# Performance work log

Hardware: AMD Instinct MI355X
Metric: run time of the kernel (lower is better)

The kernel has to match this reference:

```python
import jax, jax.numpy as jnp
import numpy as np

D0 = 1.0          # constraint distance d
NPEND = 128       # points per pendulum chain
NB = 1024         # number of chains (= batch.max()+1)
LATENT = 256      # latent dim of y
NDIM = 3          # spatial dimensions; x dim = 2*NDIM (pos + vel)


def setup_inputs() -> dict:
    key = jax.random.key(0)
    k1, k2, k3 = jax.random.split(key, 3)
    N = NB * NPEND
    y = jax.random.normal(k1, (N, LATENT), dtype=jnp.float32)
    z = jax.random.normal(k2, (N,), dtype=jnp.float32)
    K = jax.random.normal(k3, (LATENT, 2 * NDIM), dtype=jnp.float32) * 0.05
    batch = (jnp.arange(N, dtype=jnp.int32) // NPEND).astype(jnp.int32)
    return {"y": y, "z": z, "K": K, "batch": batch}


def _delta_r(r):
    # dr[:,0] = r[:,0]; dr[:,i] = r[:,i] - r[:,i-1]
    return jnp.concatenate([r[:, :1], r[:, 1:] - r[:, :-1]], axis=1)


def reference(y, z, K, batch):
    x = y @ K                                  # [N, 6]
    ndim = x.shape[-1] // 2                    # pos_only=False -> 3
    nb = batch.shape[0] // NPEND               # == batch.max()+1 by construction
    r = x[:, :ndim].reshape(nb, -1, ndim)      # [nb, npend, 3]

    dr = _delta_r(r)                           # [nb, npend, 3]
    drnorm = jnp.linalg.norm(dr, axis=-1)      # [nb, npend]
    c = drnorm - D0                            # constraint values
    rn = dr / drnorm[..., None]                # unit chain-difference vectors

    # Jacobian-transpose times constraints, fused over the chain dimension:
    # out[:,i] = c_i * rn_i - c_{i+1} * rn_{i+1};  out[:,-1] = c_{-1} * rn_{-1}
    t = c[..., None] * rn                      # [nb, npend, 3]
    out = t - jnp.concatenate([t[:, 1:], jnp.zeros_like(t[:, :1])], axis=1)

    lam_x = jnp.zeros_like(x).at[:, :ndim].set(out.reshape(-1, ndim))
    lam_y = lam_x @ K.T                        # [N, latent]
    return lam_y
```

## Files before the change

### kernel.cpp

```cpp
#include <hip/hip_runtime.h>

#define NPEND  128
#define LATENT 256
#define KCOLS  6
#define D0_C   1.0f

__global__ __launch_bounds__(256)
void pend_kernel_f32(const float* __restrict__ y,
                     const float* __restrict__ K,
                     float* __restrict__ out)
{
    __shared__ float sR[NPEND][3];

    const int tid  = threadIdx.x;
    const int wave = tid >> 6;
    const int lane = tid & 63;
    const int hw   = lane >> 5;
    const int hl   = lane & 31;

    float k0[8], k1[8], k2[8];
#pragma unroll
    for (int e = 0; e < 8; ++e) {
        const int l = hl * 8 + e;
        k0[e] = K[l * KCOLS + 0];
        k1[e] = K[l * KCOLS + 1];
        k2[e] = K[l * KCOLS + 2];
    }

    const size_t ybase = (size_t)blockIdx.x * ((size_t)NPEND * LATENT);

    for (int p = wave * 2; p < NPEND; p += 8) {
        const int row = p + hw;
        const float* yr = y + ybase + (size_t)row * LATENT + hl * 8;
        const float4 va = *(const float4*)(yr);
        const float4 vb = *(const float4*)(yr + 4);

        float s0 = va.x*k0[0] + va.y*k0[1] + va.z*k0[2] + va.w*k0[3]
                 + vb.x*k0[4] + vb.y*k0[5] + vb.z*k0[6] + vb.w*k0[7];
        float s1 = va.x*k1[0] + va.y*k1[1] + va.z*k1[2] + va.w*k1[3]
                 + vb.x*k1[4] + vb.y*k1[5] + vb.z*k1[6] + vb.w*k1[7];
        float s2 = va.x*k2[0] + va.y*k2[1] + va.z*k2[2] + va.w*k2[3]
                 + vb.x*k2[4] + vb.y*k2[5] + vb.z*k2[6] + vb.w*k2[7];

#pragma unroll
        for (int off = 16; off > 0; off >>= 1) {
            s0 += __shfl_down(s0, off, 32);
            s1 += __shfl_down(s1, off, 32);
            s2 += __shfl_down(s2, off, 32);
        }
        if (hl == 0) {
            sR[row][0] = s0; sR[row][1] = s1; sR[row][2] = s2;
        }
    }
    __syncthreads();

    for (int p = wave * 2; p < NPEND; p += 8) {
        const int row = p + hw;

        const float rx = sR[row][0], ry = sR[row][1], rz = sR[row][2];
        float px = 0.f, py = 0.f, pz = 0.f;
        if (row > 0) { px = sR[row-1][0]; py = sR[row-1][1]; pz = sR[row-1][2]; }

        const float dx = rx - px, dy = ry - py, dz = rz - pz;
        const float n  = sqrtf(dx*dx + dy*dy + dz*dz);
        const float s  = (n - D0_C) / n;
        float ox = s * dx, oy = s * dy, oz = s * dz;

        if (row < NPEND - 1) {
            const float nx = sR[row+1][0], ny = sR[row+1][1], nz = sR[row+1][2];
            const float ex = nx - rx, ey = ny - ry, ez = nz - rz;
            const float n2 = sqrtf(ex*ex + ey*ey + ez*ez);
            const float t2 = (n2 - D0_C) / n2;
            ox -= t2 * ex; oy -= t2 * ey; oz -= t2 * ez;
        }

        float4 wa, wb;
        wa.x = ox*k0[0] + oy*k1[0] + oz*k2[0];
        wa.y = ox*k0[1] + oy*k1[1] + oz*k2[1];
        wa.z = ox*k0[2] + oy*k1[2] + oz*k2[2];
        wa.w = ox*k0[3] + oy*k1[3] + oz*k2[3];
        wb.x = ox*k0[4] + oy*k1[4] + oz*k2[4];
        wb.y = ox*k0[5] + oy*k1[5] + oz*k2[5];
        wb.z = ox*k0[6] + oy*k1[6] + oz*k2[6];
        wb.w = ox*k0[7] + oy*k1[7] + oz*k2[7];

        float* orow = out + ybase + (size_t)row * LATENT + hl * 8;
        *(float4*)(orow)     = wa;
        *(float4*)(orow + 4) = wb;
    }
}

extern "C" void kernel_launch(void* const* d_in, const int* in_sizes, int n_in,
                              void* d_out, int out_size, void* d_ws, size_t ws_size,
                              hipStream_t stream) {
    const float* y = (const float*)d_in[0];
    const float* K = (const float*)d_in[2];
    float* out = (float*)d_out;

    int N  = (n_in > 1 && in_sizes) ? in_sizes[1] : (1024 * NPEND);
    int nb = N / NPEND;
    if (nb <= 0) nb = 1024;
    (void)out_size; (void)d_ws; (void)ws_size;

    pend_kernel_f32<<<nb, 256, 0, stream>>>(y, K, out);
}
```

Before: 248.3 us.

## Split each pendulum chain across four blocks with halo rows

Each block now processes a 32-row segment of a chain instead of the whole 128-row chain, and recomputes one halo row on each side to get neighbour positions. This quadruples the grid so more blocks are in flight and each block's two phases are shorter. The cost is redundant projection of up to two extra rows per segment, about six percent more reads of y.

```diff
diff --git a/kernel.cpp b/kernel.cpp
--- a/kernel.cpp
+++ b/kernel.cpp
@@ -4,19 +4,26 @@
 #define LATENT 256
 #define KCOLS  6
 #define D0_C   1.0f
+#define SEG    32
+#define SEGS_PER_CHAIN (NPEND / SEG)
 
 __global__ __launch_bounds__(256)
 void pend_kernel_f32(const float* __restrict__ y,
                      const float* __restrict__ K,
                      float* __restrict__ out)
 {
-    __shared__ float sR[NPEND][3];
+    __shared__ float sR[SEG + 2][3];
 
     const int tid  = threadIdx.x;
-    const int wave = tid >> 6;
-    const int lane = tid & 63;
-    const int hw   = lane >> 5;
-    const int hl   = lane & 31;
+    const int hwid = tid >> 5;
+    const int hl   = tid & 31;
+
+    const int chain = blockIdx.x >> 2;
+    const int seg   = blockIdx.x & 3;
+    const int row0  = seg * SEG;
+    const int rlo   = (row0 > 0) ? row0 - 1 : 0;
+    const int rhi   = (row0 + SEG < NPEND) ? row0 + SEG : NPEND - 1;
+    const int nrows = rhi - rlo + 1;
 
     float k0[8], k1[8], k2[8];
 #pragma unroll
@@ -27,11 +34,11 @@
         k2[e] = K[l * KCOLS + 2];
     }
 
-    const size_t ybase = (size_t)blockIdx.x * ((size_t)NPEND * LATENT);
+    const size_t cbase = (size_t)chain * ((size_t)NPEND * LATENT);
 
-    for (int p = wave * 2; p < NPEND; p += 8) {
-        const int row = p + hw;
-        const float* yr = y + ybase + (size_t)row * LATENT + hl * 8;
+    for (int i = hwid; i < nrows; i += 8) {
+        const int row = rlo + i;
+        const float* yr = y + cbase + (size_t)row * LATENT + hl * 8;
         const float4 va = *(const float4*)(yr);
         const float4 vb = *(const float4*)(yr + 4);
 
@@ -49,17 +56,18 @@
             s2 += __shfl_down(s2, off, 32);
         }
         if (hl == 0) {
-            sR[row][0] = s0; sR[row][1] = s1; sR[row][2] = s2;
+            sR[i][0] = s0; sR[i][1] = s1; sR[i][2] = s2;
         }
     }
     __syncthreads();
 
-    for (int p = wave * 2; p < NPEND; p += 8) {
-        const int row = p + hw;
+    for (int i = hwid; i < SEG; i += 8) {
+        const int row = row0 + i;
+        const int si  = row - rlo;
 
-        const float rx = sR[row][0], ry = sR[row][1], rz = sR[row][2];
+        const float rx = sR[si][0], ry = sR[si][1], rz = sR[si][2];
         float px = 0.f, py = 0.f, pz = 0.f;
-        if (row > 0) { px = sR[row-1][0]; py = sR[row-1][1]; pz = sR[row-1][2]; }
+        if (row > 0) { px = sR[si-1][0]; py = sR[si-1][1]; pz = sR[si-1][2]; }
 
         const float dx = rx - px, dy = ry - py, dz = rz - pz;
         const float n  = sqrtf(dx*dx + dy*dy + dz*dz);
@@ -67,7 +75,7 @@
         float ox = s * dx, oy = s * dy, oz = s * dz;
 
         if (row < NPEND - 1) {
-            const float nx = sR[row+1][0], ny = sR[row+1][1], nz = sR[row+1][2];
+            const float nx = sR[si+1][0], ny = sR[si+1][1], nz = sR[si+1][2];
             const float ex = nx - rx, ey = ny - ry, ez = nz - rz;
             const float n2 = sqrtf(ex*ex + ey*ey + ez*ez);
             const float t2 = (n2 - D0_C) / n2;
@@ -84,7 +92,7 @@
         wb.z = ox*k0[6] + oy*k1[6] + oz*k2[6];
         wb.w = ox*k0[7] + oy*k1[7] + oz*k2[7];
 
-        float* orow = out + ybase + (size_t)row * LATENT + hl * 8;
+        float* orow = out + cbase + (size_t)row * LATENT + hl * 8;
         *(float4*)(orow)     = wa;
         *(float4*)(orow + 4) = wb;
     }
@@ -102,5 +110,5 @@
     if (nb <= 0) nb = 1024;
     (void)out_size; (void)d_ws; (void)ws_size;
 
-    pend_kernel_f32<<<nb, 256, 0, stream>>>(y, K, out);
+    pend_kernel_f32<<<nb * SEGS_PER_CHAIN, 256, 0, stream>>>(y, K, out);
 }
```

Result: faster. 239.6 us (-3.5%).
